# Kernel tuning notes

Hardware: AMD Instinct MI355X
Metric: run time of the kernel (lower is better)

## Reference

```python
import jax, jax.numpy as jnp
import numpy as np

N = 50000     # nodes
E = 800000    # edges (avg degree 16)
IN = 128
HID = 128
OUT = 128


def _init_lin(key, n_out, n_in, bias=True):
    k1, k2 = jax.random.split(key)
    bound = 1.0 / np.sqrt(n_in)
    W = jax.random.uniform(k1, (n_out, n_in), minval=-bound, maxval=bound, dtype=jnp.float32)
    if bias:
        b = jax.random.uniform(k2, (n_out,), minval=-bound, maxval=bound, dtype=jnp.float32)
        return W, b
    return W


def setup_inputs() -> dict:
    key = jax.random.key(0)
    ks = jax.random.split(key, 20)
    inp = {
        "s": jax.random.normal(ks[0], (N, IN), dtype=jnp.float32),
        "t": jax.random.normal(ks[1], (N, IN), dtype=jnp.float32),
        "edge_index": jax.random.randint(ks[2], (2, E), 0, N, dtype=jnp.int64),
        "edge_weight": jax.random.normal(ks[3], (E,), dtype=jnp.float32),
    }
    dims = [(HID, IN), (OUT, HID)]
    i = 4
    for layer in range(2):
        n_out, n_in = dims[layer]
        for pre in ("s", "t"):
            Wl, bl = _init_lin(ks[i], n_out, n_in, bias=True); i += 1
            Wr = _init_lin(ks[i], n_out, n_in, bias=False); i += 1
            inp[f"{pre}{layer}_Wl"] = Wl
            inp[f"{pre}{layer}_bl"] = bl
            inp[f"{pre}{layer}_Wr"] = Wr
    return inp


def _sage(x, src, dst, w, Wl, bl, Wr):
    """SAGEConv (mean aggr, weighted messages): lin_l(mean_j w_ij x_j) + lin_r(x_i)."""
    n = x.shape[0]
    msg = x[src] * w[:, None]                                   # [E, d] gather
    agg = jax.ops.segment_sum(msg, dst, num_segments=n)         # [N, d] scatter-add
    cnt = jax.ops.segment_sum(jnp.ones_like(w), dst, num_segments=n)
    mean = agg / jnp.maximum(cnt, 1.0)[:, None]
    return mean @ Wl.T + bl + x @ Wr.T


def reference(s, t, edge_index, edge_weight,
              s0_Wl, s0_bl, s0_Wr, t0_Wl, t0_bl, t0_Wr,
              s1_Wl, s1_bl, s1_Wr, t1_Wl, t1_bl, t1_Wr):
    w = jax.nn.sigmoid(edge_weight)
    src, dst = edge_index[0], edge_index[1]
    # layer 0 (relu; dropout is identity in eval mode)
    s1 = jax.nn.relu(_sage(t, src, dst, w, s0_Wl, s0_bl, s0_Wr))
    t1 = jax.nn.relu(_sage(s, dst, src, w, t0_Wl, t0_bl, t0_Wr))  # flipped edges
    # layer 1 (no activation)
    s2 = _sage(t1, src, dst, w, s1_Wl, s1_bl, s1_Wr)
    t2 = _sage(s1, dst, src, w, t1_Wl, t1_bl, t1_Wr)
    return (s2, t2)
```

## Files before the change

### kernel.cpp

```cpp
#include <hip/hip_runtime.h>
#include <hip/hip_bf16.h>

#define DIM 128
#define BINSHIFT 8
#define BINSZ 256
#define MAXBINS2 400
#define EPB 2048
#define CAP 6144

typedef __attribute__((ext_vector_type(4))) float f32x4;
typedef __attribute__((ext_vector_type(8))) short bf16x8;
typedef __attribute__((ext_vector_type(8))) unsigned short u16x8;

static __device__ __forceinline__ float b2f(unsigned short u) {
    return __uint_as_float(((unsigned int)u) << 16);
}
static __device__ __forceinline__ unsigned short f2b(float f) {
    unsigned int x = __float_as_uint(f);
    unsigned int r = (x + 0x7fffu + ((x >> 16) & 1u)) >> 16;
    return (unsigned short)r;
}

static __device__ __forceinline__ void fma8(float* acc, float w, uint4 v) {
    const unsigned int* u = &v.x;
#pragma unroll
    for (int k = 0; k < 4; k++) {
        acc[2 * k]     += w * __uint_as_float(u[k] << 16);
        acc[2 * k + 1] += w * __uint_as_float(u[k] & 0xffff0000u);
    }
}

struct WPtrs { const float* Wl[4]; const float* Wr[4]; };

__global__ __launch_bounds__(256) void dgnn_prep(
        const float* __restrict__ s, const float* __restrict__ t,
        unsigned short* __restrict__ sb, unsigned short* __restrict__ tb,
        int n4, int cvtb, WPtrs wp, unsigned short* __restrict__ Wc, int wbase) {
    int b = blockIdx.x;
    if (b < wbase) {
        int which = (b >= cvtb) ? 1 : 0;
        int i = (b - which * cvtb) * 256 + threadIdx.x;
        if (i >= n4) return;
        const float* src = which ? t : s;
        unsigned short* dst = which ? tb : sb;
        float4 v = ((const float4*)src)[i];
        ushort4 o;
        o.x = f2b(v.x); o.y = f2b(v.y); o.z = f2b(v.z); o.w = f2b(v.w);
        ((ushort4*)dst)[i] = o;
    } else {
        int tid = (b - wbase) * 256 + threadIdx.x;
        int i4 = tid << 2;
        int conv = i4 >> 15;
        int rem = i4 & 32767;
        int ch = rem >> 8;
        int k = rem & 255;
        const float* src = (k < 128) ? wp.Wl[conv] : wp.Wr[conv];
        float4 v = *(const float4*)(src + ch * DIM + (k & 127));
        ushort4 o;
        o.x = f2b(v.x); o.y = f2b(v.y); o.z = f2b(v.z); o.w = f2b(v.w);
        *(ushort4*)(Wc + i4) = o;
    }
}

__global__ __launch_bounds__(256) void dgnn_binscatter(const float* __restrict__ ew,
        const int* __restrict__ srcI, const int* __restrict__ dstI,
        int* __restrict__ binCur, int2* __restrict__ binned, int E, int NBINS) {
    __shared__ int hist[MAXBINS2];
    const int nb2 = 2 * NBINS;
    for (int i = threadIdx.x; i < nb2; i += 256) hist[i] = 0;
    __syncthreads();
    int base = blockIdx.x * EPB;
    int end = min(base + EPB, E);
    for (int e = base + threadIdx.x; e < end; e += 256) {
        atomicAdd(&hist[dstI[e] >> BINSHIFT], 1);
        atomicAdd(&hist[NBINS + (srcI[e] >> BINSHIFT)], 1);
    }
    __syncthreads();
    for (int i = threadIdx.x; i < nb2; i += 256) {
        int c = hist[i];
        int st = c ? atomicAdd(&binCur[i], c) : 0;
        hist[i] = i * CAP + st;
    }
    __syncthreads();
    for (int e = base + threadIdx.x; e < end; e += 256) {
        int d = dstI[e], s = srcI[e];
        float x = ew[e];
        float w = 1.0f / (1.0f + expf(-x));
        int wb = __float_as_int(w);
        int packed = d | (s << 16);
        int pd = atomicAdd(&hist[d >> BINSHIFT], 1);
        binned[pd] = make_int2(packed, wb);
        int ps = atomicAdd(&hist[NBINS + (s >> BINSHIFT)], 1);
        binned[ps] = make_int2(packed, wb);
    }
}

__global__ __launch_bounds__(256) void dgnn_csrfinal(const int2* __restrict__ binned,
        const int* __restrict__ binCur,
        int* __restrict__ offsD, int* __restrict__ degD,
        int* __restrict__ offsS, int* __restrict__ degS,
        int2* __restrict__ nbr2D, int2* __restrict__ nbr2S, int N, int NBINS) {
    int b = blockIdx.x;
    bool isD = b < NBINS;
    int lb = isD ? b : b - NBINS;
    int nodeBase = lb << BINSHIFT;
    const int2* bin = binned + (size_t)b * CAP;
    int K = binCur[b]; if (K > CAP) K = CAP;
    int* offs = isD ? offsD : offsS;
    int* dga  = isD ? degD : degS;
    int2* out = (isD ? nbr2D : nbr2S) + (size_t)lb * CAP;

    __shared__ int cnt[BINSZ], cur[BINSZ], scanb[BINSZ];
    cnt[threadIdx.x] = 0;
    __syncthreads();
    for (int i = threadIdx.x; i < K; i += 256) {
        int pk = bin[i].x;
        int node = isD ? (pk & 0xffff) : ((pk >> 16) & 0xffff);
        atomicAdd(&cnt[node - nodeBase], 1);
    }
    __syncthreads();
    int v = cnt[threadIdx.x];
    scanb[threadIdx.x] = v;
    __syncthreads();
#pragma unroll
    for (int o = 1; o < 256; o <<= 1) {
        int u = (threadIdx.x >= o) ? scanb[threadIdx.x - o] : 0;
        __syncthreads();
        scanb[threadIdx.x] += u;
        __syncthreads();
    }
    int pos = scanb[threadIdx.x] - v;
    cur[threadIdx.x] = pos;
    int n = nodeBase + threadIdx.x;
    if (n < N) { offs[n] = lb * CAP + pos; dga[n] = v; }
    __syncthreads();
    for (int i = threadIdx.x; i < K; i += 256) {
        int2 en = bin[i];
        int node, nbr;
        if (isD) { node = en.x & 0xffff; nbr = (en.x >> 16) & 0xffff; }
        else     { node = (en.x >> 16) & 0xffff; nbr = en.x & 0xffff; }
        int p = atomicAdd(&cur[node - nodeBase], 1);
        out[p] = make_int2(nbr, en.y);
    }
}

__global__ __launch_bounds__(256) void dgnn_gather2(
        const unsigned short* __restrict__ xbD, const int* __restrict__ offsD,
        const int* __restrict__ degD, const int2* __restrict__ nbrD,
        unsigned short* __restrict__ meanD,
        const unsigned short* __restrict__ xbS, const int* __restrict__ offsS,
        const int* __restrict__ degS, const int2* __restrict__ nbrS,
        unsigned short* __restrict__ meanS,
        int N, int halfb) {
    int which = (blockIdx.x >= halfb) ? 1 : 0;
    const unsigned short* xb = which ? xbS : xbD;
    const int* offs          = which ? offsS : offsD;
    const int* dga           = which ? degS : degD;
    const int2* nbr2         = which ? nbrS : nbrD;
    unsigned short* meanb    = which ? meanS : meanD;

    long long gid = (long long)(blockIdx.x - which * halfb) * 256 + threadIdx.x;
    int n = (int)(gid >> 5);
    if (n >= N) return;
    const int l32 = (int)gid & 31;
    const int q2  = l32 >> 4;
    const int m   = l32 & 15;

    int beg = offs[n];
    int dg  = dga[n];
    int end = beg + dg;
    float acc[8];
#pragma unroll
    for (int k = 0; k < 8; k++) acc[k] = 0.f;

    for (int base = beg; base < end; base += 32) {
        int cnt = end - base; if (cnt > 32) cnt = 32;
        bool inb = (base + l32) < end;
        int2 gw = inb ? nbr2[base + l32] : make_int2(0, 0);
        int   g_l = gw.x;
        float w_l = __int_as_float(gw.y);

        int it = 0;
        for (; it + 16 <= cnt; it += 16) {
            int g[8]; float w[8]; uint4 v[8];
#pragma unroll
            for (int k = 0; k < 8; k++) {
                int e = it + 2 * k + q2;
                g[k] = __shfl(g_l, e, 32);
                w[k] = __shfl(w_l, e, 32);
            }
#pragma unroll
            for (int k = 0; k < 8; k++)
                v[k] = *(const uint4*)(xb + ((size_t)g[k] << 7) + (m << 3));
#pragma unroll
            for (int k = 0; k < 8; k++) fma8(acc, w[k], v[k]);
        }
        for (; it < cnt; it += 2) {
            int e0 = it + q2;
            int g0 = __shfl(g_l, e0, 32);
            float w0 = __shfl(w_l, e0, 32);
            uint4 v0 = *(const uint4*)(xb + ((size_t)g0 << 7) + (m << 3));
            fma8(acc, w0, v0);
        }
    }

#pragma unroll
    for (int k = 0; k < 8; k++)
        acc[k] += __shfl_xor(acc[k], 16);

    if (q2 == 0) {
        float inv = 1.0f / fmaxf((float)dg, 1.0f);
        u16x8 o;
#pragma unroll
        for (int k = 0; k < 8; k++) o[k] = f2b(acc[k] * inv);
        *(u16x8*)(meanb + ((size_t)n << 7) + (m << 3)) = o;
    }
}

__global__ __launch_bounds__(256) void dgnn_node2(
        const unsigned short* __restrict__ meanA, const unsigned short* __restrict__ xbA,
        const unsigned short* __restrict__ WcA, const float* __restrict__ biasA,
        float* __restrict__ outfA, unsigned short* __restrict__ outbA,
        const unsigned short* __restrict__ meanB, const unsigned short* __restrict__ xbB,
        const unsigned short* __restrict__ WcB, const float* __restrict__ biasB,
        float* __restrict__ outfB, unsigned short* __restrict__ outbB,
        int N, int mode, int halfb) {
    __shared__ __align__(16) unsigned short sW[128 * 256];

    int which = (blockIdx.x >= halfb) ? 1 : 0;
    const unsigned short* meanb = which ? meanB : meanA;
    const unsigned short* xb    = which ? xbB : xbA;
    const unsigned short* Wc    = which ? WcB : WcA;
    const float* bias           = which ? biasB : biasA;
    float* outf                 = which ? outfB : outfA;
    unsigned short* outb        = which ? outbB : outbA;
    int lb = blockIdx.x - which * halfb;

    for (int i = threadIdx.x; i < 4096; i += 256) {
        int ch = i >> 5;
        int off = (i & 31) << 4;
        float4 v = *(const float4*)((const char*)Wc + ((size_t)i << 4));
        int soff = off ^ ((ch & 7) << 4);
        *(float4*)((char*)sW + ch * 512 + soff) = v;
    }
    __syncthreads();

    const int wid = threadIdx.x >> 6;
    const int lane = threadIdx.x & 63;
    const int r = lane & 15;
    const int q = lane >> 4;
    const int ntiles = (N + 15) >> 4;

    for (int tile = lb * 4 + wid; tile < ntiles; tile += halfb * 4) {
        const int n0 = tile << 4;
        const unsigned short* A0 = meanb + (size_t)(n0 + r) * DIM + q * 8;
        const unsigned short* A1 = xb    + (size_t)(n0 + r) * DIM + q * 8;

        f32x4 acc[8];
#pragma unroll
        for (int ct = 0; ct < 8; ct++) acc[ct] = (f32x4){0.f, 0.f, 0.f, 0.f};

#pragma unroll
        for (int ks = 0; ks < 8; ks++) {
            bf16x8 a = (ks < 4) ? *(const bf16x8*)(A0 + ks * 32)
                                : *(const bf16x8*)(A1 + (ks - 4) * 32);
#pragma unroll
            for (int ct = 0; ct < 8; ct++) {
                int ch = ct * 16 + r;
                int soff = (ks * 64 + q * 16) ^ ((ch & 7) << 4);
                bf16x8 b = *(const bf16x8*)((const char*)sW + ch * 512 + soff);
                acc[ct] = __builtin_amdgcn_mfma_f32_16x16x32_bf16(a, b, acc[ct], 0, 0, 0);
            }
        }

#pragma unroll
        for (int ct = 0; ct < 8; ct++) {
            int ch = ct * 16 + r;
            float bv = bias[ch];
#pragma unroll
            for (int rr = 0; rr < 4; rr++) {
                int n = n0 + q * 4 + rr;
                if (n >= N) break;
                float v = acc[ct][rr] + bv;
                if (mode) {
                    v = fmaxf(v, 0.f);
                    outb[(size_t)n * DIM + ch] = f2b(v);
                } else {
                    outf[(size_t)n * DIM + ch] = v;
                }
            }
        }
    }
}

extern "C" void kernel_launch(void* const* d_in, const int* in_sizes, int n_in,
                              void* d_out, int out_size, void* d_ws, size_t ws_size,
                              hipStream_t stream) {
    const float* s  = (const float*)d_in[0];
    const float* t  = (const float*)d_in[1];
    const int*   ei = (const int*)d_in[2];
    const float* ew = (const float*)d_in[3];
    const float* s0_Wl = (const float*)d_in[4];
    const float* s0_bl = (const float*)d_in[5];
    const float* s0_Wr = (const float*)d_in[6];
    const float* t0_Wl = (const float*)d_in[7];
    const float* t0_bl = (const float*)d_in[8];
    const float* t0_Wr = (const float*)d_in[9];
    const float* s1_Wl = (const float*)d_in[10];
    const float* s1_bl = (const float*)d_in[11];
    const float* s1_Wr = (const float*)d_in[12];
    const float* t1_Wl = (const float*)d_in[13];
    const float* t1_bl = (const float*)d_in[14];
    const float* t1_Wr = (const float*)d_in[15];

    const int N = in_sizes[0] / DIM;
    const int E = in_sizes[3];
    const int NBINS = (N + BINSZ - 1) / BINSZ;

    int2* nbr2D = (int2*)d_ws;
    int2* nbr2S = nbr2D + (size_t)NBINS * CAP;
    unsigned short* up = (unsigned short*)(nbr2S + (size_t)NBINS * CAP);
    unsigned short* sb    = up;
    unsigned short* tb    = sb    + (size_t)N * DIM;
    unsigned short* meanA = tb    + (size_t)N * DIM;
    unsigned short* meanB = meanA + (size_t)N * DIM;
    unsigned short* s1b   = meanB + (size_t)N * DIM;
    unsigned short* t1b   = s1b   + (size_t)N * DIM;
    unsigned short* Wc    = t1b   + (size_t)N * DIM;
    int* ip     = (int*)(Wc + 4 * 128 * 256);
    int* binCur = ip;
    int* offsD  = binCur + 2 * NBINS;
    int* degD   = offsD + N;
    int* offsS  = degD + N;
    int* degS   = offsS + N;

    int2* binned = (int2*)meanA;

    float* sout = (float*)d_out;
    float* tout = sout + (size_t)N * DIM;

    const int* srcI = ei;
    const int* dstI = ei + E;

    const int binb = (E + EPB - 1) / EPB;
    const int gbH = (int)(((long long)N * 32 + 255) / 256);
    const int nodeb = 256;
    const int cvtb = ((N * DIM / 4) + 255) / 256;

    WPtrs wp;
    wp.Wl[0] = s0_Wl; wp.Wr[0] = s0_Wr;
    wp.Wl[1] = t0_Wl; wp.Wr[1] = t0_Wr;
    wp.Wl[2] = s1_Wl; wp.Wr[2] = s1_Wr;
    wp.Wl[3] = t1_Wl; wp.Wr[3] = t1_Wr;
    hipMemsetAsync(binCur, 0, (size_t)2 * NBINS * sizeof(int), stream);
    dgnn_prep<<<2 * cvtb + 128, 256, 0, stream>>>(s, t, sb, tb, N * DIM / 4,
                                                  cvtb, wp, Wc, 2 * cvtb);

    dgnn_binscatter<<<binb, 256, 0, stream>>>(ew, srcI, dstI, binCur, binned, E, NBINS);
    dgnn_csrfinal<<<2 * NBINS, 256, 0, stream>>>(binned, binCur,
                                                 offsD, degD, offsS, degS,
                                                 nbr2D, nbr2S, N, NBINS);

    dgnn_gather2<<<2 * gbH, 256, 0, stream>>>(tb, offsD, degD, nbr2D, meanA,
                                              sb, offsS, degS, nbr2S, meanB, N, gbH);
    dgnn_node2<<<2 * nodeb, 256, 0, stream>>>(
        meanA, tb, Wc,         s0_bl, nullptr, s1b,
        meanB, sb, Wc + 32768, t0_bl, nullptr, t1b, N, 1, nodeb);

    dgnn_gather2<<<2 * gbH, 256, 0, stream>>>(t1b, offsD, degD, nbr2D, meanA,
                                              s1b, offsS, degS, nbr2S, meanB, N, gbH);
    dgnn_node2<<<2 * nodeb, 256, 0, stream>>>(
        meanA, t1b, Wc + 2 * 32768, s1_bl, sout, nullptr,
        meanB, s1b, Wc + 3 * 32768, t1_bl, tout, nullptr, N, 0, nodeb);
}
```

Before: 253.3 us.

## Switch to fp16 storage, pack neighbor index+fp16 weight, use fdot2 gather

Node features, weights and the intermediate means move from bf16 to fp16, and the GEMM switches to the f16 MFMA. Each CSR neighbor entry is packed into 32 bits: a 16-bit index plus an fp16 edge weight. This halves the neighbor-list traffic in the gather. The gather loop now processes 4 neighbors per step, using perm to pair two neighbors' values and v_dot2 to accumulate into fp32. Costs are reduced fp16 range and precision, and fewer loads in flight per iteration, which may weaken latency hiding.

Result: faster. 233.0 us (-8.0%).

```diff
diff --git a/kernel.cpp b/kernel.cpp
--- a/kernel.cpp
+++ b/kernel.cpp
@@ -9,26 +9,24 @@
 #define CAP 6144
 
 typedef __attribute__((ext_vector_type(4))) float f32x4;
-typedef __attribute__((ext_vector_type(8))) short bf16x8;
+typedef __attribute__((ext_vector_type(8))) _Float16 h16x8;
+typedef __attribute__((ext_vector_type(2))) _Float16 h16x2;
 typedef __attribute__((ext_vector_type(8))) unsigned short u16x8;
 
-static __device__ __forceinline__ float b2f(unsigned short u) {
-    return __uint_as_float(((unsigned int)u) << 16);
-}
-static __device__ __forceinline__ unsigned short f2b(float f) {
-    unsigned int x = __float_as_uint(f);
-    unsigned int r = (x + 0x7fffu + ((x >> 16) & 1u)) >> 16;
-    return (unsigned short)r;
-}
-
-static __device__ __forceinline__ void fma8(float* acc, float w, uint4 v) {
-    const unsigned int* u = &v.x;
-#pragma unroll
-    for (int k = 0; k < 4; k++) {
-        acc[2 * k]     += w * __uint_as_float(u[k] << 16);
-        acc[2 * k + 1] += w * __uint_as_float(u[k] & 0xffff0000u);
-    }
-}
+static __device__ __forceinline__ unsigned short f2h(float f) {
+    _Float16 h = (_Float16)f;
+    return __builtin_bit_cast(unsigned short, h);
+}
+
+#if __has_builtin(__builtin_amdgcn_fdot2)
+static __device__ __forceinline__ float dot2(h16x2 a, h16x2 b, float c) {
+    return __builtin_amdgcn_fdot2(a, b, c, false);
+}
+#else
+static __device__ __forceinline__ float dot2(h16x2 a, h16x2 b, float c) {
+    return c + (float)a.x * (float)b.x + (float)a.y * (float)b.y;
+}
+#endif
 
 struct WPtrs { const float* Wl[4]; const float* Wr[4]; };
 
@@ -45,7 +43,7 @@
         unsigned short* dst = which ? tb : sb;
         float4 v = ((const float4*)src)[i];
         ushort4 o;
-        o.x = f2b(v.x); o.y = f2b(v.y); o.z = f2b(v.z); o.w = f2b(v.w);
+        o.x = f2h(v.x); o.y = f2h(v.y); o.z = f2h(v.z); o.w = f2h(v.w);
         ((ushort4*)dst)[i] = o;
     } else {
         int tid = (b - wbase) * 256 + threadIdx.x;
@@ -57,7 +55,7 @@
         const float* src = (k < 128) ? wp.Wl[conv] : wp.Wr[conv];
         float4 v = *(const float4*)(src + ch * DIM + (k & 127));
         ushort4 o;
-        o.x = f2b(v.x); o.y = f2b(v.y); o.z = f2b(v.z); o.w = f2b(v.w);
+        o.x = f2h(v.x); o.y = f2h(v.y); o.z = f2h(v.z); o.w = f2h(v.w);
         *(ushort4*)(Wc + i4) = o;
     }
 }
@@ -99,7 +97,8 @@
         const int* __restrict__ binCur,
         int* __restrict__ offsD, int* __restrict__ degD,
         int* __restrict__ offsS, int* __restrict__ degS,
-        int2* __restrict__ nbr2D, int2* __restrict__ nbr2S, int N, int NBINS) {
+        unsigned int* __restrict__ nbrPD, unsigned int* __restrict__ nbrPS,
+        int N, int NBINS) {
     int b = blockIdx.x;
     bool isD = b < NBINS;
     int lb = isD ? b : b - NBINS;
@@ -108,7 +107,7 @@
     int K = binCur[b]; if (K > CAP) K = CAP;
     int* offs = isD ? offsD : offsS;
     int* dga  = isD ? degD : degS;
-    int2* out = (isD ? nbr2D : nbr2S) + (size_t)lb * CAP;
+    unsigned int* out = (isD ? nbrPD : nbrPS) + (size_t)lb * CAP;
 
     __shared__ int cnt[BINSZ], cur[BINSZ], scanb[BINSZ];
     cnt[threadIdx.x] = 0;
@@ -140,23 +139,24 @@
         if (isD) { node = en.x & 0xffff; nbr = (en.x >> 16) & 0xffff; }
         else     { node = (en.x >> 16) & 0xffff; nbr = en.x & 0xffff; }
         int p = atomicAdd(&cur[node - nodeBase], 1);
-        out[p] = make_int2(nbr, en.y);
-    }
-}
-
-__global__ __launch_bounds__(256) void dgnn_gather2(
+        unsigned short wh = f2h(__int_as_float(en.y));
+        out[p] = (unsigned int)nbr | ((unsigned int)wh << 16);
+    }
+}
+
+__global__ __launch_bounds__(256, 8) void dgnn_gather2(
         const unsigned short* __restrict__ xbD, const int* __restrict__ offsD,
-        const int* __restrict__ degD, const int2* __restrict__ nbrD,
+        const int* __restrict__ degD, const unsigned int* __restrict__ nbrD,
         unsigned short* __restrict__ meanD,
         const unsigned short* __restrict__ xbS, const int* __restrict__ offsS,
-        const int* __restrict__ degS, const int2* __restrict__ nbrS,
+        const int* __restrict__ degS, const unsigned int* __restrict__ nbrS,
         unsigned short* __restrict__ meanS,
         int N, int halfb) {
     int which = (blockIdx.x >= halfb) ? 1 : 0;
     const unsigned short* xb = which ? xbS : xbD;
     const int* offs          = which ? offsS : offsD;
     const int* dga           = which ? degS : degD;
-    const int2* nbr2         = which ? nbrS : nbrD;
+    const unsigned int* nbrP = which ? nbrS : nbrD;
     unsigned short* meanb    = which ? meanS : meanD;
 
     long long gid = (long long)(blockIdx.x - which * halfb) * 256 + threadIdx.x;
@@ -176,31 +176,41 @@
     for (int base = beg; base < end; base += 32) {
         int cnt = end - base; if (cnt > 32) cnt = 32;
         bool inb = (base + l32) < end;
-        int2 gw = inb ? nbr2[base + l32] : make_int2(0, 0);
-        int   g_l = gw.x;
-        float w_l = __int_as_float(gw.y);
-
-        int it = 0;
-        for (; it + 16 <= cnt; it += 16) {
-            int g[8]; float w[8]; uint4 v[8];
-#pragma unroll
-            for (int k = 0; k < 8; k++) {
-                int e = it + 2 * k + q2;
-                g[k] = __shfl(g_l, e, 32);
-                w[k] = __shfl(w_l, e, 32);
+        unsigned int pk_l = inb ? nbrP[base + l32] : 0u;
+
+        for (int it = 0; it < cnt; it += 8) {
+            int e0 = it + (q2 << 1);
+            unsigned int p00 = __shfl(pk_l, e0, 32);
+            unsigned int p01 = __shfl(pk_l, e0 + 1, 32);
+            unsigned int p10 = __shfl(pk_l, e0 + 4, 32);
+            unsigned int p11 = __shfl(pk_l, e0 + 5, 32);
+            uint4 v00 = *(const uint4*)(xb + ((size_t)(p00 & 0xffffu) << 7) + (m << 3));
+            uint4 v01 = *(const uint4*)(xb + ((size_t)(p01 & 0xffffu) << 7) + (m << 3));
+            uint4 v10 = *(const uint4*)(xb + ((size_t)(p10 & 0xffffu) << 7) + (m << 3));
+            uint4 v11 = *(const uint4*)(xb + ((size_t)(p11 & 0xffffu) << 7) + (m << 3));
+            h16x2 wp0 = __builtin_bit_cast(h16x2,
+                __builtin_amdgcn_perm(p01, p00, 0x07060302u));
+            h16x2 wp1 = __builtin_bit_cast(h16x2,
+                __builtin_amdgcn_perm(p11, p10, 0x07060302u));
+            const unsigned int* u0 = &v00.x;
+            const unsigned int* u1 = &v01.x;
+            const unsigned int* u2 = &v10.x;
+            const unsigned int* u3 = &v11.x;
+#pragma unroll
+            for (int k = 0; k < 4; k++) {
+                h16x2 lo0 = __builtin_bit_cast(h16x2,
+                    __builtin_amdgcn_perm(u1[k], u0[k], 0x05040100u));
+                h16x2 hi0 = __builtin_bit_cast(h16x2,
+                    __builtin_amdgcn_perm(u1[k], u0[k], 0x07060302u));
+                acc[2 * k]     = dot2(wp0, lo0, acc[2 * k]);
+                acc[2 * k + 1] = dot2(wp0, hi0, acc[2 * k + 1]);
+                h16x2 lo1 = __builtin_bit_cast(h16x2,
+                    __builtin_amdgcn_perm(u3[k], u2[k], 0x05040100u));
+                h16x2 hi1 = __builtin_bit_cast(h16x2,
+                    __builtin_amdgcn_perm(u3[k], u2[k], 0x07060302u));
+                acc[2 * k]     = dot2(wp1, lo1, acc[2 * k]);
+                acc[2 * k + 1] = dot2(wp1, hi1, acc[2 * k + 1]);
             }
-#pragma unroll
-            for (int k = 0; k < 8; k++)
-                v[k] = *(const uint4*)(xb + ((size_t)g[k] << 7) + (m << 3));
-#pragma unroll
-            for (int k = 0; k < 8; k++) fma8(acc, w[k], v[k]);
-        }
-        for (; it < cnt; it += 2) {
-            int e0 = it + q2;
-            int g0 = __shfl(g_l, e0, 32);
-            float w0 = __shfl(w_l, e0, 32);
-            uint4 v0 = *(const uint4*)(xb + ((size_t)g0 << 7) + (m << 3));
-            fma8(acc, w0, v0);
         }
     }
 
@@ -212,7 +222,7 @@
         float inv = 1.0f / fmaxf((float)dg, 1.0f);
         u16x8 o;
 #pragma unroll
-        for (int k = 0; k < 8; k++) o[k] = f2b(acc[k] * inv);
+        for (int k = 0; k < 8; k++) o[k] = f2h(acc[k] * inv);
         *(u16x8*)(meanb + ((size_t)n << 7) + (m << 3)) = o;
     }
 }
@@ -262,14 +272,14 @@
 
 #pragma unroll
         for (int ks = 0; ks < 8; ks++) {
-            bf16x8 a = (ks < 4) ? *(const bf16x8*)(A0 + ks * 32)
-                                : *(const bf16x8*)(A1 + (ks - 4) * 32);
+            h16x8 a = (ks < 4) ? *(const h16x8*)(A0 + ks * 32)
+                               : *(const h16x8*)(A1 + (ks - 4) * 32);
 #pragma unroll
             for (int ct = 0; ct < 8; ct++) {
                 int ch = ct * 16 + r;
                 int soff = (ks * 64 + q * 16) ^ ((ch & 7) << 4);
-                bf16x8 b = *(const bf16x8*)((const char*)sW + ch * 512 + soff);
-                acc[ct] = __builtin_amdgcn_mfma_f32_16x16x32_bf16(a, b, acc[ct], 0, 0, 0);
+                h16x8 b = *(const h16x8*)((const char*)sW + ch * 512 + soff);
+                acc[ct] = __builtin_amdgcn_mfma_f32_16x16x32_f16(a, b, acc[ct], 0, 0, 0);
             }
         }
 
@@ -284,7 +294,7 @@
                 float v = acc[ct][rr] + bv;
                 if (mode) {
                     v = fmaxf(v, 0.f);
-                    outb[(size_t)n * DIM + ch] = f2b(v);
+                    outb[(size_t)n * DIM + ch] = f2h(v);
                 } else {
                     outf[(size_t)n * DIM + ch] = v;
                 }
@@ -317,9 +327,9 @@
     const int E = in_sizes[3];
     const int NBINS = (N + BINSZ - 1) / BINSZ;
 
-    int2* nbr2D = (int2*)d_ws;
-    int2* nbr2S = nbr2D + (size_t)NBINS * CAP;
-    unsigned short* up = (unsigned short*)(nbr2S + (size_t)NBINS * CAP);
+    unsigned int* nbrPD = (unsigned int*)d_ws;
+    unsigned int* nbrPS = nbrPD + (size_t)NBINS * CAP;
+    unsigned short* up = (unsigned short*)(nbrPS + (size_t)NBINS * CAP);
     unsigned short* sb    = up;
     unsigned short* tb    = sb    + (size_t)N * DIM;
     unsigned short* meanA = tb    + (size_t)N * DIM;
@@ -359,16 +369,16 @@
     dgnn_binscatter<<<binb, 256, 0, stream>>>(ew, srcI, dstI, binCur, binned, E, NBINS);
     dgnn_csrfinal<<<2 * NBINS, 256, 0, stream>>>(binned, binCur,
                                                  offsD, degD, offsS, degS,
-                                                 nbr2D, nbr2S, N, NBINS);
-
-    dgnn_gather2<<<2 * gbH, 256, 0, stream>>>(tb, offsD, degD, nbr2D, meanA,
-                                              sb, offsS, degS, nbr2S, meanB, N, gbH);
+                                                 nbrPD, nbrPS, N, NBINS);
+
+    dgnn_gather2<<<2 * gbH, 256, 0, stream>>>(tb, offsD, degD, nbrPD, meanA,
+                                              sb, offsS, degS, nbrPS, meanB, N, gbH);
     dgnn_node2<<<2 * nodeb, 256, 0, stream>>>(
         meanA, tb, Wc,         s0_bl, nullptr, s1b,
         meanB, sb, Wc + 32768, t0_bl, nullptr, t1b, N, 1, nodeb);
 
-    dgnn_gather2<<<2 * gbH, 256, 0, stream>>>(t1b, offsD, degD, nbr2D, meanA,
-                                              s1b, offsS, degS, nbr2S, meanB, N, gbH);
+    dgnn_gather2<<<2 * gbH, 256, 0, stream>>>(t1b, offsD, degD, nbrPD, meanA,
+                                              s1b, offsS, degS, nbrPS, meanB, N, gbH);
     dgnn_node2<<<2 * nodeb, 256, 0, stream>>>(
         meanA, t1b, Wc + 2 * 32768, s1_bl, sout, nullptr,
         meanB, s1b, Wc + 3 * 32768, t1_bl, tout, nullptr, N, 0, nodeb);
```
